# Performance work log

Hardware: AMD Instinct MI355X
Metric: run time of the kernel (lower is better)

## Reference

```python
import jax, jax.numpy as jnp
import numpy as np

N_NODES = 100000
N_EDGES = 1600000
N_FEAT = 128
HIDDEN = 16
EMBED = 128
N_GRAPHS = 64


def setup_inputs() -> dict:
    key = jax.random.key(0)
    ks = jax.random.split(key, 6)
    x = jax.random.normal(ks[0], (N_NODES, N_FEAT), dtype=jnp.float32)
    edge_index = jax.random.randint(ks[1], (2, N_EDGES), 0, N_NODES, dtype=jnp.int32)
    batch = jnp.sort(jax.random.randint(ks[2], (N_NODES,), 0, N_GRAPHS, dtype=jnp.int32))
    W1 = jax.random.normal(ks[3], (N_FEAT, HIDDEN), dtype=jnp.float32) * (1.0 / np.sqrt(N_FEAT))
    b1 = jnp.zeros((HIDDEN,), dtype=jnp.float32)
    W2 = jax.random.normal(ks[4], (HIDDEN, EMBED), dtype=jnp.float32) * (1.0 / np.sqrt(HIDDEN))
    b2 = jnp.zeros((EMBED,), dtype=jnp.float32)
    return {"x": x, "edge_index": edge_index, "batch": batch,
            "W1": W1, "b1": b1, "W2": W2, "b2": b2}


def _gcn_conv(x, W, b, src, dst, dinv):
    # x' = D^{-1/2} (A + I) D^{-1/2} (x W) + b ; (src, dst) already include self-loops
    h = x @ W                                   # [N, out]
    norm = dinv[src] * dinv[dst]                # [E']
    msg = h[src] * norm[:, None]                # gather + scale
    out = jax.ops.segment_sum(msg, dst, num_segments=x.shape[0])  # scatter-add
    return out + b


def reference(x, edge_index, batch, W1, b1, W2, b2):
    n = x.shape[0]
    loop = jnp.arange(n, dtype=edge_index.dtype)
    src = jnp.concatenate([edge_index[0], loop])  # add self-loops
    dst = jnp.concatenate([edge_index[1], loop])
    deg = jax.ops.segment_sum(jnp.ones_like(dst, dtype=x.dtype), dst, num_segments=n)
    dinv = jnp.where(deg > 0, jax.lax.rsqrt(deg), 0.0)

    h = _gcn_conv(x, W1, b1, src, dst, dinv)
    h = jax.nn.relu(h)
    # dropout(p=0.2) is identity in eval mode
    h = _gcn_conv(h, W2, b2, src, dst, dinv)

    # mean pooling over graphs in the batch
    sums = jax.ops.segment_sum(h, batch, num_segments=N_GRAPHS)          # [G, EMBED]
    cnt = jax.ops.segment_sum(jnp.ones((n,), dtype=h.dtype), batch, num_segments=N_GRAPHS)
    return sums / jnp.maximum(cnt, 1.0)[:, None]
```

## Files before the change

### kernel.cpp

```cpp
#include <hip/hip_runtime.h>

#define HIDDEN 16
#define N_FEAT 128
#define EMBED 128
#define N_GRAPHS 64
#define BSH 8
#define MAXB 512
#define EPT 8

typedef unsigned int uint;

__device__ inline uint pk2(float a, float b) {
    uint ua = __float_as_uint(a), ub = __float_as_uint(b);
    ua = (ua + 0x7FFFu + ((ua >> 16) & 1u)) >> 16;
    ub = (ub + 0x7FFFu + ((ub >> 16) & 1u)) & 0xFFFF0000u;
    return ua | ub;
}
__device__ inline float2 upk2(uint w) {
    return make_float2(__uint_as_float(w << 16), __uint_as_float(w & 0xFFFF0000u));
}

__global__ void __launch_bounds__(1024)
k_hist(const int* __restrict__ dst, int n_edges, int nbuck, int* __restrict__ ghist) {
    __shared__ int h[MAXB];
    for (int i = threadIdx.x; i < MAXB; i += 1024) h[i] = 0;
    __syncthreads();
    int base = blockIdx.x * (EPT * 1024);
#pragma unroll
    for (int j = 0; j < EPT; j++) {
        int e = base + j * 1024 + threadIdx.x;
        if (e < n_edges) atomicAdd(&h[dst[e] >> BSH], 1);
    }
    __syncthreads();
    for (int b = threadIdx.x; b < nbuck; b += 1024)
        if (h[b]) atomicAdd(&ghist[b], h[b]);
}

__global__ void k_scan(const int* __restrict__ ghist, int nbuck,
                       int* __restrict__ gbase, int* __restrict__ gfill) {
    __shared__ int s[MAXB];
    int t = threadIdx.x;
    s[t] = (t < nbuck) ? ghist[t] : 0;
    __syncthreads();
    for (int st = 1; st < MAXB; st <<= 1) {
        int v = (t >= st) ? s[t - st] : 0;
        __syncthreads();
        s[t] += v;
        __syncthreads();
    }
    if (t < nbuck) {
        int excl = s[t] - ghist[t];
        gbase[t] = excl;
        gfill[t] = excl;
    }
}

__global__ void __launch_bounds__(1024)
k_part(const int* __restrict__ src, const int* __restrict__ dst,
       int n_edges, int nbuck, int* __restrict__ gfill, uint* __restrict__ ebuf) {
    __shared__ int hcnt[MAXB];
    __shared__ int hincl[MAXB];
    __shared__ int hrank[MAXB];
    __shared__ int hbase[MAXB];
    __shared__ uint stage[EPT * 1024];
    __shared__ unsigned short sbuck[EPT * 1024];
    int tid = threadIdx.x;
    for (int i = tid; i < MAXB; i += 1024) { hcnt[i] = 0; hrank[i] = 0; }
    __syncthreads();
    int base = blockIdx.x * (EPT * 1024);
    int cnt = min(EPT * 1024, n_edges - base);
    int s_[EPT], d_[EPT];
#pragma unroll
    for (int j = 0; j < EPT; j++) {
        int k = j * 1024 + tid;
        if (k < cnt) {
            s_[j] = src[base + k]; d_[j] = dst[base + k];
            atomicAdd(&hcnt[d_[j] >> BSH], 1);
        }
    }
    __syncthreads();
    if (tid < MAXB) hincl[tid] = hcnt[tid];
    __syncthreads();
    for (int st = 1; st < MAXB; st <<= 1) {
        int v = 0;
        if (tid < MAXB && tid >= st) v = hincl[tid - st];
        __syncthreads();
        if (tid < MAXB) hincl[tid] += v;
        __syncthreads();
    }
    if (tid < nbuck && hcnt[tid] > 0)
        hbase[tid] = atomicAdd(&gfill[tid], hcnt[tid]);
    __syncthreads();
#pragma unroll
    for (int j = 0; j < EPT; j++) {
        int k = j * 1024 + tid;
        if (k < cnt) {
            int b = d_[j] >> BSH;
            int r = atomicAdd(&hrank[b], 1);
            int pos = hincl[b] - hcnt[b] + r;
            stage[pos] = ((uint)s_[j] << 8) | ((uint)d_[j] & 255u);
            sbuck[pos] = (unsigned short)b;
        }
    }
    __syncthreads();
    for (int t = tid; t < cnt; t += 1024) {
        int b = sbuck[t];
        ebuf[hbase[b] + (t - (hincl[b] - hcnt[b]))] = stage[t];
    }
}

__global__ void __launch_bounds__(1024)
k_csr(const uint* __restrict__ ebuf, const int* __restrict__ gbase,
      const int* __restrict__ ghist, int n,
      int* __restrict__ deg, int* __restrict__ rowp, int* __restrict__ col) {
    __shared__ int nh[256], nincl[256], nrank[256];
    int b = blockIdx.x;
    int tid = threadIdx.x;
    int seg0 = gbase[b];
    int cnt = ghist[b];
    int nb0 = b << BSH;
    if (tid < 256) { nh[tid] = 0; nrank[tid] = 0; }
    __syncthreads();
    for (int t = tid; t < cnt; t += 1024)
        atomicAdd(&nh[ebuf[seg0 + t] & 255u], 1);
    __syncthreads();
    if (tid < 256) nincl[tid] = nh[tid];
    __syncthreads();
    for (int st = 1; st < 256; st <<= 1) {
        int v = 0;
        if (tid < 256 && tid >= st) v = nincl[tid - st];
        __syncthreads();
        if (tid < 256) nincl[tid] += v;
        __syncthreads();
    }
    if (tid < 256) {
        int node = nb0 + tid;
        if (node < n) {
            deg[node]  = nh[tid];
            rowp[node] = seg0 + nincl[tid] - nh[tid];
        }
    }
    __syncthreads();
    for (int t = tid; t < cnt; t += 1024) {
        uint e = ebuf[seg0 + t];
        int ln = (int)(e & 255u);
        int r = atomicAdd(&nrank[ln], 1);
        col[seg0 + (nincl[ln] - nh[ln]) + r] = (int)(e >> 8);
    }
}

__global__ void k_gemm1(const float* __restrict__ x, const float* __restrict__ W1,
                        const int* __restrict__ deg, float* __restrict__ dinv,
                        uint* __restrict__ Hs2, int n) {
    __shared__ float Ws[N_FEAT * HIDDEN];
    int tid = threadIdx.x;
    {
        const float4* w4 = (const float4*)W1;
        float4* s4 = (float4*)Ws;
        s4[tid * 2]     = w4[tid * 2];
        s4[tid * 2 + 1] = w4[tid * 2 + 1];
    }
    __syncthreads();
    int i = blockIdx.x * blockDim.x + tid;
    if (i >= n) return;

    float acc[HIDDEN];
#pragma unroll
    for (int o = 0; o < HIDDEN; o++) acc[o] = 0.f;

    const float4* xr = (const float4*)(x + (size_t)i * N_FEAT);
#pragma unroll 8
    for (int k4 = 0; k4 < N_FEAT / 4; k4++) {
        float4 xv = xr[k4];
        const float* w0 = &Ws[(k4 * 4 + 0) * HIDDEN];
        const float* w1 = &Ws[(k4 * 4 + 1) * HIDDEN];
        const float* w2 = &Ws[(k4 * 4 + 2) * HIDDEN];
        const float* w3 = &Ws[(k4 * 4 + 3) * HIDDEN];
#pragma unroll
        for (int o = 0; o < HIDDEN; o++)
            acc[o] += xv.x * w0[o] + xv.y * w1[o] + xv.z * w2[o] + xv.w * w3[o];
    }
    float di = rsqrtf((float)deg[i] + 1.0f);
    dinv[i] = di;
    uint o8[8];
#pragma unroll
    for (int j = 0; j < 8; j++) o8[j] = pk2(acc[2 * j] * di, acc[2 * j + 1] * di);
    uint4* hp = (uint4*)(Hs2 + (size_t)i * 8);
    hp[0] = make_uint4(o8[0], o8[1], o8[2], o8[3]);
    hp[1] = make_uint4(o8[4], o8[5], o8[6], o8[7]);
}

template <int LAYER>
__global__ void k_pull(const uint* __restrict__ V2, const int* __restrict__ rowptr,
                       const int* __restrict__ deg, const int* __restrict__ col,
                       const float* __restrict__ dinv, const float* __restrict__ b1,
                       uint* __restrict__ out2, int n) {
    int wid = (blockIdx.x * blockDim.x + threadIdx.x) >> 6;
    int lane = threadIdx.x & 63;
    if (wid >= n) return;
    int f  = lane & 7;
    int es = lane >> 3;
    int start = rowptr[wid];
    int dg = deg[wid];
    float ax = 0.f, ay = 0.f;
    for (int j = es; j < dg; j += 8) {
        int s = col[start + j];
        float2 v = upk2(V2[(size_t)s * 8 + f]);
        ax += v.x; ay += v.y;
    }
    ax += __shfl_xor(ax, 8, 64);  ay += __shfl_xor(ay, 8, 64);
    ax += __shfl_xor(ax, 16, 64); ay += __shfl_xor(ay, 16, 64);
    ax += __shfl_xor(ax, 32, 64); ay += __shfl_xor(ay, 32, 64);
    if (lane < 8) {
        float2 h = upk2(V2[(size_t)wid * 8 + f]);
        float tx = ax + h.x, ty = ay + h.y;
        float di = dinv[wid];
        if (LAYER == 1) {
            float qa = fmaxf(di * tx + b1[2 * f],     0.f) * di;
            float qb = fmaxf(di * ty + b1[2 * f + 1], 0.f) * di;
            out2[(size_t)wid * 8 + f] = pk2(qa, qb);
        } else {
            out2[(size_t)wid * 8 + f] = pk2(di * tx, di * ty);
        }
    }
}

__global__ void k_pool(const uint* __restrict__ R2, const int* __restrict__ batch,
                       float* __restrict__ S, float* __restrict__ cnt, int n) {
    __shared__ float ls[8 * HIDDEN];
    __shared__ float lc[8];
    int tid = threadIdx.x;
    if (tid < 8) lc[tid] = 0.f;
    if (tid < 8 * HIDDEN) ls[tid] = 0.f;
    __syncthreads();

    int i0 = blockIdx.x * 256;
    int g0 = batch[i0 < n ? i0 : (n - 1)];
    int i = i0 + tid;
    if (i < n) {
        int g = batch[i];
        float r[HIDDEN];
#pragma unroll
        for (int j = 0; j < 8; j++) {
            float2 v = upk2(R2[(size_t)i * 8 + j]);
            r[2 * j] = v.x; r[2 * j + 1] = v.y;
        }
        int off = g - g0;
        if (off >= 0 && off < 8) {
#pragma unroll
            for (int o = 0; o < HIDDEN; o++) atomicAdd(&ls[off * HIDDEN + o], r[o]);
            atomicAdd(&lc[off], 1.f);
        } else {
#pragma unroll
            for (int o = 0; o < HIDDEN; o++) atomicAdd(&S[(size_t)g * HIDDEN + o], r[o]);
            atomicAdd(&cnt[g], 1.f);
        }
    }
    __syncthreads();
    if (tid < 8 * HIDDEN) {
        int b = tid >> 4, o = tid & 15;
        int g = g0 + b;
        float v = ls[b * HIDDEN + o];
        if (v != 0.f && g < N_GRAPHS) atomicAdd(&S[(size_t)g * HIDDEN + o], v);
    }
    if (tid < 8) {
        int g = g0 + tid;
        float c = lc[tid];
        if (c != 0.f && g < N_GRAPHS) atomicAdd(&cnt[g], c);
    }
}

__global__ void k_out(const float* __restrict__ S, const float* __restrict__ cnt,
                      const float* __restrict__ W2, const float* __restrict__ b2,
                      float* __restrict__ out) {
    int g = blockIdx.x;
    int e = threadIdx.x;
    float c = cnt[g];
    float acc = 0.f;
#pragma unroll
    for (int k = 0; k < HIDDEN; k++) acc += S[g * HIDDEN + k] * W2[k * EMBED + e];
    out[g * EMBED + e] = (c > 0.f) ? (acc / c + b2[e]) : 0.f;
}

extern "C" void kernel_launch(void* const* d_in, const int* in_sizes, int n_in,
                              void* d_out, int out_size, void* d_ws, size_t ws_size,
                              hipStream_t stream) {
    const float* x     = (const float*)d_in[0];
    const int*   ei    = (const int*)  d_in[1];
    const int*   batch = (const int*)  d_in[2];
    const float* W1    = (const float*)d_in[3];
    const float* b1    = (const float*)d_in[4];
    const float* W2    = (const float*)d_in[5];
    const float* b2    = (const float*)d_in[6];
    float* out = (float*)d_out;

    const int n       = in_sizes[2];
    const int n_edges = in_sizes[1] / 2;
    const int* srcp = ei;
    const int* dstp = ei + n_edges;
    const int nbuck = (n + 255) >> BSH;

    uint*  Hs2   = (uint*)d_ws;
    uint*  Q2    = Hs2 + (size_t)n * 8;
    float* dinv  = (float*)(Q2 + (size_t)n * 8);
    int*   deg   = (int*)(dinv + n);
    int*   rowp  = deg + n;
    int*   col   = rowp + n;
    uint*  ebuf  = (uint*)(col + n_edges);
    int*   ghist = (int*)(ebuf + n_edges);
    float* S     = (float*)(ghist + MAXB);
    float* cnt   = S + N_GRAPHS * HIDDEN;
    int*   gbase = (int*)(cnt + N_GRAPHS);
    int*   gfill = gbase + MAXB;
    uint*  R2    = ebuf;

    hipMemsetAsync(ghist, 0, (MAXB + N_GRAPHS * HIDDEN + N_GRAPHS) * sizeof(int), stream);

    const int pb8k = (n_edges + EPT * 1024 - 1) / (EPT * 1024);
    k_hist <<<pb8k, 1024, 0, stream>>>(dstp, n_edges, nbuck, ghist);
    k_scan <<<1, MAXB, 0, stream>>>(ghist, nbuck, gbase, gfill);
    k_part <<<pb8k, 1024, 0, stream>>>(srcp, dstp, n_edges, nbuck, gfill, ebuf);
    k_csr  <<<nbuck, 1024, 0, stream>>>(ebuf, gbase, ghist, n, deg, rowp, col);

    const int nb = (n + 255) / 256;
    k_gemm1<<<nb, 256, 0, stream>>>(x, W1, deg, dinv, Hs2, n);

    const int pullb = (n * 64 + 255) / 256;
    k_pull<1><<<pullb, 256, 0, stream>>>(Hs2, rowp, deg, col, dinv, b1, Q2, n);
    k_pull<2><<<pullb, 256, 0, stream>>>(Q2,  rowp, deg, col, dinv, b1, R2, n);

    k_pool <<<nb, 256, 0, stream>>>(R2, batch, S, cnt, n);
    k_out  <<<N_GRAPHS, EMBED, 0, stream>>>(S, cnt, W2, b2, out);
}
```

Before: 242.4 us.

## Merge CSR build passes via per-slice partition table and last-block tickets

```diff
diff --git a/kernel.cpp b/kernel.cpp
--- a/kernel.cpp
+++ b/kernel.cpp
@@ -6,7 +6,8 @@
 #define N_GRAPHS 64
 #define BSH 8
 #define MAXB 512
-#define EPT 8
+#define ESL 8192
+#define NSMAX 256
 
 typedef unsigned int uint;
 
@@ -19,59 +20,29 @@
 __device__ inline float2 upk2(uint w) {
     return make_float2(__uint_as_float(w << 16), __uint_as_float(w & 0xFFFF0000u));
 }
+__device__ inline int aload(const int* p) {
+    return __hip_atomic_load(p, __ATOMIC_RELAXED, __HIP_MEMORY_SCOPE_AGENT);
+}
+__device__ inline float aloadf(const float* p) {
+    return __hip_atomic_load(p, __ATOMIC_RELAXED, __HIP_MEMORY_SCOPE_AGENT);
+}
 
 __global__ void __launch_bounds__(1024)
-k_hist(const int* __restrict__ dst, int n_edges, int nbuck, int* __restrict__ ghist) {
-    __shared__ int h[MAXB];
-    for (int i = threadIdx.x; i < MAXB; i += 1024) h[i] = 0;
-    __syncthreads();
-    int base = blockIdx.x * (EPT * 1024);
-#pragma unroll
-    for (int j = 0; j < EPT; j++) {
-        int e = base + j * 1024 + threadIdx.x;
-        if (e < n_edges) atomicAdd(&h[dst[e] >> BSH], 1);
-    }
-    __syncthreads();
-    for (int b = threadIdx.x; b < nbuck; b += 1024)
-        if (h[b]) atomicAdd(&ghist[b], h[b]);
-}
-
-__global__ void k_scan(const int* __restrict__ ghist, int nbuck,
-                       int* __restrict__ gbase, int* __restrict__ gfill) {
-    __shared__ int s[MAXB];
-    int t = threadIdx.x;
-    s[t] = (t < nbuck) ? ghist[t] : 0;
-    __syncthreads();
-    for (int st = 1; st < MAXB; st <<= 1) {
-        int v = (t >= st) ? s[t - st] : 0;
-        __syncthreads();
-        s[t] += v;
-        __syncthreads();
-    }
-    if (t < nbuck) {
-        int excl = s[t] - ghist[t];
-        gbase[t] = excl;
-        gfill[t] = excl;
-    }
-}
-
-__global__ void __launch_bounds__(1024)
-k_part(const int* __restrict__ src, const int* __restrict__ dst,
-       int n_edges, int nbuck, int* __restrict__ gfill, uint* __restrict__ ebuf) {
-    __shared__ int hcnt[MAXB];
-    __shared__ int hincl[MAXB];
-    __shared__ int hrank[MAXB];
-    __shared__ int hbase[MAXB];
-    __shared__ uint stage[EPT * 1024];
-    __shared__ unsigned short sbuck[EPT * 1024];
+k_part2(const int* __restrict__ src, const int* __restrict__ dst,
+        int n_edges, int nbuck,
+        uint* __restrict__ ebuf, uint* __restrict__ ptab,
+        int* __restrict__ ghist, int* __restrict__ gbase, int* __restrict__ ticket) {
+    __shared__ int hcnt[MAXB], hincl[MAXB], hrank[MAXB];
+    __shared__ uint stage[ESL];
+    __shared__ int amLast;
     int tid = threadIdx.x;
     for (int i = tid; i < MAXB; i += 1024) { hcnt[i] = 0; hrank[i] = 0; }
     __syncthreads();
-    int base = blockIdx.x * (EPT * 1024);
-    int cnt = min(EPT * 1024, n_edges - base);
-    int s_[EPT], d_[EPT];
-#pragma unroll
-    for (int j = 0; j < EPT; j++) {
+    int base = blockIdx.x * ESL;
+    int cnt = min(ESL, n_edges - base);
+    int s_[8], d_[8];
+#pragma unroll
+    for (int j = 0; j < 8; j++) {
         int k = j * 1024 + tid;
         if (k < cnt) {
             s_[j] = src[base + k]; d_[j] = dst[base + k];
@@ -88,41 +59,76 @@
         if (tid < MAXB) hincl[tid] += v;
         __syncthreads();
     }
-    if (tid < nbuck && hcnt[tid] > 0)
-        hbase[tid] = atomicAdd(&gfill[tid], hcnt[tid]);
-    __syncthreads();
-#pragma unroll
-    for (int j = 0; j < EPT; j++) {
+    if (tid < MAXB) {
+        int c = hcnt[tid];
+        ptab[(size_t)tid * NSMAX + blockIdx.x] = ((uint)(hincl[tid] - c) << 16) | (uint)c;
+        if (c) atomicAdd(&ghist[tid], c);
+    }
+    __syncthreads();
+#pragma unroll
+    for (int j = 0; j < 8; j++) {
         int k = j * 1024 + tid;
         if (k < cnt) {
             int b = d_[j] >> BSH;
             int r = atomicAdd(&hrank[b], 1);
-            int pos = hincl[b] - hcnt[b] + r;
-            stage[pos] = ((uint)s_[j] << 8) | ((uint)d_[j] & 255u);
-            sbuck[pos] = (unsigned short)b;
-        }
-    }
-    __syncthreads();
-    for (int t = tid; t < cnt; t += 1024) {
-        int b = sbuck[t];
-        ebuf[hbase[b] + (t - (hincl[b] - hcnt[b]))] = stage[t];
+            stage[hincl[b] - hcnt[b] + r] = ((uint)s_[j] << 8) | ((uint)d_[j] & 255u);
+        }
+    }
+    __syncthreads();
+    for (int t = tid; t < cnt; t += 1024) ebuf[base + t] = stage[t];
+    __threadfence();
+    __syncthreads();
+    if (tid == 0) amLast = (atomicAdd(ticket, 1) == (int)gridDim.x - 1);
+    __syncthreads();
+    if (amLast) {
+        int v = 0;
+        if (tid < MAXB) { v = aload(&ghist[tid]); hcnt[tid] = v; hincl[tid] = v; }
+        __syncthreads();
+        for (int st = 1; st < MAXB; st <<= 1) {
+            int u = 0;
+            if (tid < MAXB && tid >= st) u = hincl[tid - st];
+            __syncthreads();
+            if (tid < MAXB) hincl[tid] += u;
+            __syncthreads();
+        }
+        if (tid < MAXB) gbase[tid] = hincl[tid] - hcnt[tid];
     }
 }
 
 __global__ void __launch_bounds__(1024)
-k_csr(const uint* __restrict__ ebuf, const int* __restrict__ gbase,
-      const int* __restrict__ ghist, int n,
-      int* __restrict__ deg, int* __restrict__ rowp, int* __restrict__ col) {
+k_csr2(const uint* __restrict__ ebuf, const uint* __restrict__ ptab,
+       const int* __restrict__ gbase, int nslice, int n,
+       int* __restrict__ rowp, float* __restrict__ dinv, int* __restrict__ col) {
+    __shared__ uint eL[ESL];
+    __shared__ int coff[NSMAX];
     __shared__ int nh[256], nincl[256], nrank[256];
-    int b = blockIdx.x;
-    int tid = threadIdx.x;
-    int seg0 = gbase[b];
-    int cnt = ghist[b];
-    int nb0 = b << BSH;
+    int b = blockIdx.x, tid = threadIdx.x, nb0 = b << BSH;
+    int ccnt = 0;
+    if (tid < nslice) ccnt = (int)(ptab[(size_t)b * NSMAX + tid] & 0xFFFFu);
+    if (tid < NSMAX) coff[tid] = ccnt;
+    __syncthreads();
+    for (int st = 1; st < NSMAX; st <<= 1) {
+        int v = 0;
+        if (tid < NSMAX && tid >= st) v = coff[tid - st];
+        __syncthreads();
+        if (tid < NSMAX) coff[tid] += v;
+        __syncthreads();
+    }
+    int total = coff[NSMAX - 1];
+    if (total > ESL) total = ESL;
+    int wv = tid >> 6, ln = tid & 63;
+    for (int s = wv; s < nslice; s += 16) {
+        uint pe = ptab[(size_t)b * NSMAX + s];
+        int off = (int)(pe >> 16), c = (int)(pe & 0xFFFFu);
+        int cbase = coff[s] - c;
+        for (int i = ln; i < c && (cbase + i) < ESL; i += 64)
+            eL[cbase + i] = ebuf[(size_t)s * ESL + off + i];
+    }
+    __syncthreads();
     if (tid < 256) { nh[tid] = 0; nrank[tid] = 0; }
     __syncthreads();
-    for (int t = tid; t < cnt; t += 1024)
-        atomicAdd(&nh[ebuf[seg0 + t] & 255u], 1);
+    for (int t = tid; t < total; t += 1024)
+        atomicAdd(&nh[eL[t] & 255u], 1);
     __syncthreads();
     if (tid < 256) nincl[tid] = nh[tid];
     __syncthreads();
@@ -133,25 +139,29 @@
         if (tid < 256) nincl[tid] += v;
         __syncthreads();
     }
+    int g0 = gbase[b];
     if (tid < 256) {
         int node = nb0 + tid;
         if (node < n) {
-            deg[node]  = nh[tid];
-            rowp[node] = seg0 + nincl[tid] - nh[tid];
-        }
-    }
-    __syncthreads();
-    for (int t = tid; t < cnt; t += 1024) {
-        uint e = ebuf[seg0 + t];
-        int ln = (int)(e & 255u);
-        int r = atomicAdd(&nrank[ln], 1);
-        col[seg0 + (nincl[ln] - nh[ln]) + r] = (int)(e >> 8);
+            rowp[node] = g0 + nincl[tid] - nh[tid];
+            dinv[node] = rsqrtf((float)nh[tid] + 1.0f);
+        }
+        if (tid == 0) {
+            int e = nb0 + 256; if (e > n) e = n;
+            rowp[e] = g0 + total;
+        }
+    }
+    __syncthreads();
+    for (int t = tid; t < total; t += 1024) {
+        uint e = eL[t];
+        int l2 = (int)(e & 255u);
+        int r = atomicAdd(&nrank[l2], 1);
+        col[g0 + (nincl[l2] - nh[l2]) + r] = (int)(e >> 8);
     }
 }
 
 __global__ void k_gemm1(const float* __restrict__ x, const float* __restrict__ W1,
-                        const int* __restrict__ deg, float* __restrict__ dinv,
-                        uint* __restrict__ Hs2, int n) {
+                        const float* __restrict__ dinv, uint* __restrict__ Hs2, int n) {
     __shared__ float Ws[N_FEAT * HIDDEN];
     int tid = threadIdx.x;
     {
@@ -180,8 +190,7 @@
         for (int o = 0; o < HIDDEN; o++)
             acc[o] += xv.x * w0[o] + xv.y * w1[o] + xv.z * w2[o] + xv.w * w3[o];
     }
-    float di = rsqrtf((float)deg[i] + 1.0f);
-    dinv[i] = di;
+    float di = dinv[i];
     uint o8[8];
 #pragma unroll
     for (int j = 0; j < 8; j++) o8[j] = pk2(acc[2 * j] * di, acc[2 * j + 1] * di);
@@ -191,19 +200,27 @@
 }
 
 template <int LAYER>
-__global__ void k_pull(const uint* __restrict__ V2, const int* __restrict__ rowptr,
-                       const int* __restrict__ deg, const int* __restrict__ col,
-                       const float* __restrict__ dinv, const float* __restrict__ b1,
-                       uint* __restrict__ out2, int n) {
+__global__ void k_pull(const uint* __restrict__ V2, const int* __restrict__ rowp,
+                       const int* __restrict__ col, const float* __restrict__ dinv,
+                       const float* __restrict__ b1, uint* __restrict__ out2, int n) {
     int wid = (blockIdx.x * blockDim.x + threadIdx.x) >> 6;
     int lane = threadIdx.x & 63;
     if (wid >= n) return;
     int f  = lane & 7;
     int es = lane >> 3;
-    int start = rowptr[wid];
-    int dg = deg[wid];
+    int start = rowp[wid];
+    int dg = rowp[wid + 1] - start;
     float ax = 0.f, ay = 0.f;
-    for (int j = es; j < dg; j += 8) {
+    int c0 = -1, c1 = -1, c2 = -1, c3 = -1;
+    if (es      < dg) c0 = col[start + es];
+    if (es + 8  < dg) c1 = col[start + es + 8];
+    if (es + 16 < dg) c2 = col[start + es + 16];
+    if (es + 24 < dg) c3 = col[start + es + 24];
+    if (c0 >= 0) { float2 v = upk2(V2[(size_t)c0 * 8 + f]); ax += v.x; ay += v.y; }
+    if (c1 >= 0) { float2 v = upk2(V2[(size_t)c1 * 8 + f]); ax += v.x; ay += v.y; }
+    if (c2 >= 0) { float2 v = upk2(V2[(size_t)c2 * 8 + f]); ax += v.x; ay += v.y; }
+    if (c3 >= 0) { float2 v = upk2(V2[(size_t)c3 * 8 + f]); ax += v.x; ay += v.y; }
+    for (int j = es + 32; j < dg; j += 8) {
         int s = col[start + j];
         float2 v = upk2(V2[(size_t)s * 8 + f]);
         ax += v.x; ay += v.y;
@@ -226,9 +243,14 @@
 }
 
 __global__ void k_pool(const uint* __restrict__ R2, const int* __restrict__ batch,
-                       float* __restrict__ S, float* __restrict__ cnt, int n) {
+                       const float* __restrict__ W2, const float* __restrict__ b2,
+                       float* __restrict__ S, float* __restrict__ cnt,
+                       int* __restrict__ ticket, float* __restrict__ out, int n) {
     __shared__ float ls[8 * HIDDEN];
     __shared__ float lc[8];
+    __shared__ float Ssh[N_GRAPHS * HIDDEN];
+    __shared__ float csh[N_GRAPHS];
+    __shared__ int amLast;
     int tid = threadIdx.x;
     if (tid < 8) lc[tid] = 0.f;
     if (tid < 8 * HIDDEN) ls[tid] = 0.f;
@@ -258,9 +280,9 @@
     }
     __syncthreads();
     if (tid < 8 * HIDDEN) {
-        int b = tid >> 4, o = tid & 15;
-        int g = g0 + b;
-        float v = ls[b * HIDDEN + o];
+        int bb = tid >> 4, o = tid & 15;
+        int g = g0 + bb;
+        float v = ls[bb * HIDDEN + o];
         if (v != 0.f && g < N_GRAPHS) atomicAdd(&S[(size_t)g * HIDDEN + o], v);
     }
     if (tid < 8) {
@@ -268,18 +290,23 @@
         float c = lc[tid];
         if (c != 0.f && g < N_GRAPHS) atomicAdd(&cnt[g], c);
     }
-}
-
-__global__ void k_out(const float* __restrict__ S, const float* __restrict__ cnt,
-                      const float* __restrict__ W2, const float* __restrict__ b2,
-                      float* __restrict__ out) {
-    int g = blockIdx.x;
-    int e = threadIdx.x;
-    float c = cnt[g];
-    float acc = 0.f;
-#pragma unroll
-    for (int k = 0; k < HIDDEN; k++) acc += S[g * HIDDEN + k] * W2[k * EMBED + e];
-    out[g * EMBED + e] = (c > 0.f) ? (acc / c + b2[e]) : 0.f;
+    __threadfence();
+    __syncthreads();
+    if (tid == 0) amLast = (atomicAdd(ticket, 1) == (int)gridDim.x - 1);
+    __syncthreads();
+    if (amLast) {
+        for (int k = tid; k < N_GRAPHS * HIDDEN; k += 256) Ssh[k] = aloadf(&S[k]);
+        for (int k = tid; k < N_GRAPHS; k += 256) csh[k] = aloadf(&cnt[k]);
+        __syncthreads();
+        for (int idx = tid; idx < N_GRAPHS * EMBED; idx += 256) {
+            int g = idx >> 7, e = idx & 127;
+            float c = csh[g];
+            float acc = 0.f;
+#pragma unroll
+            for (int k = 0; k < HIDDEN; k++) acc += Ssh[g * HIDDEN + k] * W2[k * EMBED + e];
+            out[idx] = (c > 0.f) ? (acc / c + b2[e]) : 0.f;
+        }
+    }
 }
 
 extern "C" void kernel_launch(void* const* d_in, const int* in_sizes, int n_in,
@@ -298,37 +325,36 @@
     const int n_edges = in_sizes[1] / 2;
     const int* srcp = ei;
     const int* dstp = ei + n_edges;
-    const int nbuck = (n + 255) >> BSH;
+    const int nbuck  = (n + 255) >> BSH;
+    const int nslice = (n_edges + ESL - 1) / ESL;
 
     uint*  Hs2   = (uint*)d_ws;
     uint*  Q2    = Hs2 + (size_t)n * 8;
     float* dinv  = (float*)(Q2 + (size_t)n * 8);
-    int*   deg   = (int*)(dinv + n);
-    int*   rowp  = deg + n;
-    int*   col   = rowp + n;
+    int*   rowp  = (int*)(dinv + n);
+    int*   col   = rowp + (n + 2);
     uint*  ebuf  = (uint*)(col + n_edges);
-    int*   ghist = (int*)(ebuf + n_edges);
-    float* S     = (float*)(ghist + MAXB);
+    uint*  ptab  = ebuf + n_edges;
+    int*   ghist = (int*)(ptab + (size_t)MAXB * NSMAX);
+    int*   gbase = ghist + MAXB;
+    float* S     = (float*)(gbase + MAXB);
     float* cnt   = S + N_GRAPHS * HIDDEN;
-    int*   gbase = (int*)(cnt + N_GRAPHS);
-    int*   gfill = gbase + MAXB;
+    int*   tks   = (int*)(cnt + N_GRAPHS);
     uint*  R2    = ebuf;
 
-    hipMemsetAsync(ghist, 0, (MAXB + N_GRAPHS * HIDDEN + N_GRAPHS) * sizeof(int), stream);
-
-    const int pb8k = (n_edges + EPT * 1024 - 1) / (EPT * 1024);
-    k_hist <<<pb8k, 1024, 0, stream>>>(dstp, n_edges, nbuck, ghist);
-    k_scan <<<1, MAXB, 0, stream>>>(ghist, nbuck, gbase, gfill);
-    k_part <<<pb8k, 1024, 0, stream>>>(srcp, dstp, n_edges, nbuck, gfill, ebuf);
-    k_csr  <<<nbuck, 1024, 0, stream>>>(ebuf, gbase, ghist, n, deg, rowp, col);
+    hipMemsetAsync(ghist, 0,
+                   (MAXB + MAXB + N_GRAPHS * HIDDEN + N_GRAPHS + 4) * sizeof(int), stream);
+
+    k_part2<<<nslice, 1024, 0, stream>>>(srcp, dstp, n_edges, nbuck,
+                                         ebuf, ptab, ghist, gbase, tks);
+    k_csr2 <<<nbuck, 1024, 0, stream>>>(ebuf, ptab, gbase, nslice, n, rowp, dinv, col);
 
     const int nb = (n + 255) / 256;
-    k_gemm1<<<nb, 256, 0, stream>>>(x, W1, deg, dinv, Hs2, n);
+    k_gemm1<<<nb, 256, 0, stream>>>(x, W1, dinv, Hs2, n);
 
     const int pullb = (n * 64 + 255) / 256;
-    k_pull<1><<<pullb, 256, 0, stream>>>(Hs2, rowp, deg, col, dinv, b1, Q2, n);
-    k_pull<2><<<pullb, 256, 0, stream>>>(Q2,  rowp, deg, col, dinv, b1, R2, n);
-
-    k_pool <<<nb, 256, 0, stream>>>(R2, batch, S, cnt, n);
-    k_out  <<<N_GRAPHS, EMBED, 0, stream>>>(S, cnt, W2, b2, out);
-}
+    k_pull<1><<<pullb, 256, 0, stream>>>(Hs2, rowp, col, dinv, b1, Q2, n);
+    k_pull<2><<<pullb, 256, 0, stream>>>(Q2,  rowp, col, dinv, b1, R2, n);
+
+    k_pool <<<nb, 256, 0, stream>>>(R2, batch, W2, b2, S, cnt, tks + 1, out, n);
+}
```

Result: slower. 325.3 us (+34.2%).
